# Optimization experiments

Hardware: AMD Instinct MI355X
Metric: run time of the kernel (lower is better)

Reference implementation:

```python
import jax, jax.numpy as jnp
import numpy as np

N = 50000
E = 800000
IN_DIM, HID, HEADS, OUT_DIM = 32, 64, 4, 128
HC = HID * HEADS  # 256
LN_EPS = 1e-5
NEG_SLOPE = 0.2


def setup_inputs() -> dict:
    key = jax.random.key(0)
    ks = jax.random.split(key, 16)
    s = 0.05
    inp = {
        "x": jax.random.normal(ks[0], (N, IN_DIM), dtype=jnp.float32),
        "edge_index": jax.random.randint(ks[1], (2, E), 0, N, dtype=jnp.int32),
        # input projection
        "W_in": jax.random.normal(ks[2], (IN_DIM, HID), dtype=jnp.float32) * s,
        "b_in": jnp.zeros((HID,), dtype=jnp.float32),
        # GAT layer 0: in=HID, out=HID per head, HEADS heads
        "lin0_w": jax.random.normal(ks[3], (HID, HC), dtype=jnp.float32) * s,
        "att0_src": jax.random.normal(ks[4], (HEADS, HID), dtype=jnp.float32) * s,
        "att0_dst": jax.random.normal(ks[5], (HEADS, HID), dtype=jnp.float32) * s,
        "bias0": jnp.zeros((HC,), dtype=jnp.float32),
        # GAT layer 1: in=HC, out=HID per head
        "lin1_w": jax.random.normal(ks[6], (HC, HC), dtype=jnp.float32) * s,
        "att1_src": jax.random.normal(ks[7], (HEADS, HID), dtype=jnp.float32) * s,
        "att1_dst": jax.random.normal(ks[8], (HEADS, HID), dtype=jnp.float32) * s,
        "bias1": jnp.zeros((HC,), dtype=jnp.float32),
        # output projection + layernorm
        "W_out": jax.random.normal(ks[9], (HC, OUT_DIM), dtype=jnp.float32) * s,
        "b_out": jnp.zeros((OUT_DIM,), dtype=jnp.float32),
        "ln_gamma": jnp.ones((OUT_DIM,), dtype=jnp.float32),
        "ln_beta": jnp.zeros((OUT_DIM,), dtype=jnp.float32),
    }
    return inp


def _gat_conv(x, src, dst, lin_w, att_src, att_dst, bias):
    # x: [N, F_in]; src/dst: [E'] (self-loops included)
    h = (x @ lin_w).reshape(N, HEADS, HID)           # [N, H, C]
    a_src = jnp.einsum("nhc,hc->nh", h, att_src)      # [N, H]
    a_dst = jnp.einsum("nhc,hc->nh", h, att_dst)      # [N, H]
    e = a_src[src] + a_dst[dst]                        # [E', H]
    e = jnp.where(e > 0, e, NEG_SLOPE * e)             # leaky_relu(0.2)
    # segment softmax over incoming edges per destination
    m = jax.ops.segment_max(e, dst, num_segments=N)    # [N, H]
    p = jnp.exp(e - m[dst])
    denom = jax.ops.segment_sum(p, dst, num_segments=N)
    alpha = p / (denom[dst] + 1e-16)                   # [E', H]
    msg = h[src] * alpha[:, :, None]                   # [E', H, C]
    out = jax.ops.segment_sum(msg, dst, num_segments=N)  # [N, H, C]
    return out.reshape(N, HC) + bias


def reference(x, edge_index, W_in, b_in, lin0_w, att0_src, att0_dst, bias0,
              lin1_w, att1_src, att1_dst, bias1, W_out, b_out, ln_gamma, ln_beta):
    # add self-loops (PyG GATConv default)
    loops = jnp.arange(N, dtype=edge_index.dtype)
    src = jnp.concatenate([edge_index[0], loops])
    dst = jnp.concatenate([edge_index[1], loops])

    h = jax.nn.elu(x @ W_in + b_in)
    h = jax.nn.elu(_gat_conv(h, src, dst, lin0_w, att0_src, att0_dst, bias0))
    h = jax.nn.elu(_gat_conv(h, src, dst, lin1_w, att1_src, att1_dst, bias1))
    h = h @ W_out + b_out
    mu = jnp.mean(h, axis=-1, keepdims=True)
    var = jnp.mean((h - mu) ** 2, axis=-1, keepdims=True)
    return (h - mu) * jax.lax.rsqrt(var + LN_EPS) * ln_gamma + ln_beta
```

## Files before the change

kernel.cpp:

```cpp
#include <hip/hip_runtime.h>
#include <cstdint>

#define N_NODES 50000
#define N_EDGES 800000
#define EP (N_EDGES + N_NODES)
#define IN_DIM 32
#define HID 64
#define HEADS 4
#define HC 256
#define OUT_DIM 128
#define NEG_SLOPE 0.2f
#define LN_EPS 1e-5f
#define SCAN_B 1024
#define NB ((N_NODES + SCAN_B - 1) / SCAN_B)

typedef __attribute__((ext_vector_type(8))) short bf16x8;
typedef __attribute__((ext_vector_type(16))) float f32x16;

__device__ __forceinline__ unsigned bf16rne(float f) {
    unsigned u = __float_as_uint(f);
    return (u + 0x7fffu + ((u >> 16) & 1u)) >> 16;
}
__device__ __forceinline__ unsigned pack_bf2(float a, float b) {
    return bf16rne(a) | (bf16rne(b) << 16);
}
__device__ __forceinline__ float bf_lo(unsigned w) { return __uint_as_float(w << 16); }
__device__ __forceinline__ float bf_hi(unsigned w) { return __uint_as_float(w & 0xffff0000u); }

__global__ void k_in_proj(const float* __restrict__ x, const float* __restrict__ W,
                          const float* __restrict__ b, unsigned short* __restrict__ out) {
    int g = blockIdx.x * blockDim.x + threadIdx.x;
    int n = g >> 6, j = g & 63;
    const float* xr = x + n * IN_DIM;
    float acc = b[j];
#pragma unroll
    for (int k = 0; k < IN_DIM; ++k) acc += xr[k] * W[k * HID + j];
    acc = acc > 0.f ? acc : (__expf(acc) - 1.f);
    out[g] = (unsigned short)bf16rne(acc);
}

__global__ void k_wpack(const float* __restrict__ w0, const float* __restrict__ w1,
                        const float* __restrict__ w2, unsigned short* __restrict__ p0,
                        unsigned short* __restrict__ p1, unsigned short* __restrict__ p2) {
    int g = blockIdx.x * blockDim.x + threadIdx.x;
    if (g < HID * HC) {
        int k = g >> 8, n = g & 255;
        p0[(((k >> 3) * HC) + n) * 8 + (k & 7)] = (unsigned short)bf16rne(w0[g]);
    } else if (g < HID * HC + HC * HC) {
        int t = g - HID * HC;
        int k = t >> 8, n = t & 255;
        p1[(((k >> 3) * HC) + n) * 8 + (k & 7)] = (unsigned short)bf16rne(w1[t]);
    } else if (g < HID * HC + HC * HC + HC * OUT_DIM) {
        int t = g - HID * HC - HC * HC;
        int k = t >> 7, n = t & 127;
        p2[(((k >> 3) * OUT_DIM) + n) * 8 + (k & 7)] = (unsigned short)bf16rne(w2[t]);
    }
}

__global__ void k_att_w(const float* __restrict__ w, const float* __restrict__ as,
                        const float* __restrict__ ad, unsigned short* __restrict__ ext,
                        int K) {
    int t = blockIdx.x * blockDim.x + threadIdx.x;
    if (t >= K * 8) return;
    int k = t >> 3, col = t & 7, h = col & 3;
    const float* att = (col < 4) ? as : ad;
    float acc = 0.f;
#pragma unroll 4
    for (int c = 0; c < HID; ++c) acc += w[k * HC + h * HID + c] * att[h * HID + c];
    ext[(k >> 3) * 256 + col * 8 + (k & 7)] = (unsigned short)bf16rne(acc);
}

template <int K>
__global__ __launch_bounds__(256) void k_gemm_lin(
        const unsigned short* __restrict__ A, const unsigned short* __restrict__ Bp,
        const unsigned short* __restrict__ Ext, unsigned short* __restrict__ hh,
        float* __restrict__ a_src, float* __restrict__ a_dst) {
    const int lane = threadIdx.x & 63;
    const int quad = lane >> 5, c = lane & 31;
    const int wave = threadIdx.x >> 6;
    const int m0 = blockIdx.x * 64 + (wave >> 1) * 32;
    const int cb = (wave & 1) * 128;
    f32x16 acc[4];
#pragma unroll
    for (int nt = 0; nt < 4; ++nt)
#pragma unroll
        for (int i = 0; i < 16; ++i) acc[nt][i] = 0.f;
    f32x16 acce;
#pragma unroll
    for (int i = 0; i < 16; ++i) acce[i] = 0.f;
    int mrow = m0 + c; if (mrow >= N_NODES) mrow = N_NODES - 1;
    const size_t abase = (size_t)mrow * K + quad * 8;
    for (int k0 = 0; k0 < K; k0 += 16) {
        bf16x8 af = *(const bf16x8*)(A + abase + k0);
        const unsigned short* bk = Bp + ((size_t)(k0 >> 3) + quad) * (HC * 8);
#pragma unroll
        for (int nt = 0; nt < 4; ++nt) {
            bf16x8 bf = *(const bf16x8*)(bk + (cb + nt * 32 + c) * 8);
            acc[nt] = __builtin_amdgcn_mfma_f32_32x32x16_bf16(af, bf, acc[nt], 0, 0, 0);
        }
        if (wave & 1) {
            bf16x8 bfe = *(const bf16x8*)(Ext + ((k0 >> 3) + quad) * 256 + c * 8);
            acce = __builtin_amdgcn_mfma_f32_32x32x16_bf16(af, bfe, acce, 0, 0, 0);
        }
    }
#pragma unroll
    for (int reg = 0; reg < 16; ++reg) {
        int row = (reg & 3) + 8 * (reg >> 2) + 4 * quad;
        int m = m0 + row;
        if (m < N_NODES) {
            size_t base = (size_t)m * HC + cb + c;
#pragma unroll
            for (int nt = 0; nt < 4; ++nt)
                hh[base + nt * 32] = (unsigned short)bf16rne(acc[nt][reg]);
            if ((wave & 1) && c < 8) {
                float v = acce[reg];
                if (c < 4) a_src[m * HEADS + c] = v;
                else       a_dst[m * HEADS + (c - 4)] = v;
            }
        }
    }
}

__global__ void k_hist(const int* __restrict__ ei, int* __restrict__ counts,
                       int* __restrict__ rank) {
    int e = blockIdx.x * blockDim.x + threadIdx.x;
    if (e >= EP) return;
    int d = (e < N_EDGES) ? ei[N_EDGES + e] : (e - N_EDGES);
    rank[e] = atomicAdd(&counts[d], 1);
}

__global__ void k_scan1(const int* __restrict__ counts, int* __restrict__ chunk_excl,
                        int* __restrict__ bsum) {
    __shared__ int buf[SCAN_B];
    int i = blockIdx.x * SCAN_B + threadIdx.x;
    int v = (i < N_NODES) ? counts[i] : 0;
    buf[threadIdx.x] = v;
    __syncthreads();
    for (int off = 1; off < SCAN_B; off <<= 1) {
        int t = (threadIdx.x >= off) ? buf[threadIdx.x - off] : 0;
        __syncthreads();
        buf[threadIdx.x] += t;
        __syncthreads();
    }
    if (i < N_NODES) chunk_excl[i] = buf[threadIdx.x] - v;
    if (threadIdx.x == SCAN_B - 1) bsum[blockIdx.x] = buf[SCAN_B - 1];
}

__global__ void k_scan3(const int* __restrict__ chunk_excl, const int* __restrict__ bsum,
                        int* __restrict__ row_ptr) {
    __shared__ int sbase;
    if (threadIdx.x < 64) {
        int v = (threadIdx.x < blockIdx.x) ? bsum[threadIdx.x] : 0;
#pragma unroll
        for (int mk = 1; mk < 64; mk <<= 1) v += __shfl_xor(v, mk, 64);
        if (threadIdx.x == 0) sbase = v;
    }
    __syncthreads();
    int i = blockIdx.x * SCAN_B + threadIdx.x;
    if (i < N_NODES) row_ptr[i] = chunk_excl[i] + sbase;
    if (i == 0) row_ptr[N_NODES] = EP;
}

__global__ void k_scatter(const int* __restrict__ ei, const int* __restrict__ row_ptr,
                          const int* __restrict__ rank, int* __restrict__ esrc) {
    int e = blockIdx.x * blockDim.x + threadIdx.x;
    if (e >= EP) return;
    int s, d;
    if (e < N_EDGES) { s = ei[e]; d = ei[N_EDGES + e]; } else { s = d = e - N_EDGES; }
    esrc[row_ptr[d] + rank[e]] = s;
}

__global__ __launch_bounds__(256) void k_gat_agg(
        const int* __restrict__ row_ptr, const int* __restrict__ esrc,
        const unsigned short* __restrict__ hh, const float* __restrict__ a_src,
        const float* __restrict__ a_dst, const float* __restrict__ bias,
        unsigned short* __restrict__ out) {
    const int wave = threadIdx.x >> 6;
    const int lane = threadIdx.x & 63;
    const int d = blockIdx.x * 4 + wave;
    const int h = lane >> 4;
    const unsigned j = (unsigned)(lane * 4);
    const float ad = a_dst[((unsigned)d << 2) + h];
    const int beg = row_ptr[d], end = row_ptr[d + 1];
    float4 acc = {0.f, 0.f, 0.f, 0.f};
    float psum = 0.f;
    for (int base = beg; base < end; base += 64) {
        int cnt = end - base; if (cnt > 64) cnt = 64;
        int idx = base + lane;
        int myv = esrc[idx < end ? idx : end - 1];
        int i = 0;
        for (; i + 8 <= cnt; i += 8) {
            int s0 = __shfl(myv, i, 64),     s1 = __shfl(myv, i + 1, 64);
            int s2 = __shfl(myv, i + 2, 64), s3 = __shfl(myv, i + 3, 64);
            int s4 = __shfl(myv, i + 4, 64), s5 = __shfl(myv, i + 5, 64);
            int s6 = __shfl(myv, i + 6, 64), s7 = __shfl(myv, i + 7, 64);
            float as0 = a_src[((unsigned)s0 << 2) + h], as1 = a_src[((unsigned)s1 << 2) + h];
            float as2 = a_src[((unsigned)s2 << 2) + h], as3 = a_src[((unsigned)s3 << 2) + h];
            float as4 = a_src[((unsigned)s4 << 2) + h], as5 = a_src[((unsigned)s5 << 2) + h];
            float as6 = a_src[((unsigned)s6 << 2) + h], as7 = a_src[((unsigned)s7 << 2) + h];
            uint2 g0 = *(const uint2*)(hh + (((unsigned)s0 << 8) + j));
            uint2 g1 = *(const uint2*)(hh + (((unsigned)s1 << 8) + j));
            uint2 g2 = *(const uint2*)(hh + (((unsigned)s2 << 8) + j));
            uint2 g3 = *(const uint2*)(hh + (((unsigned)s3 << 8) + j));
            uint2 g4 = *(const uint2*)(hh + (((unsigned)s4 << 8) + j));
            uint2 g5 = *(const uint2*)(hh + (((unsigned)s5 << 8) + j));
            uint2 g6 = *(const uint2*)(hh + (((unsigned)s6 << 8) + j));
            uint2 g7 = *(const uint2*)(hh + (((unsigned)s7 << 8) + j));
            float e0 = as0 + ad, e1 = as1 + ad, e2 = as2 + ad, e3 = as3 + ad;
            float e4 = as4 + ad, e5 = as5 + ad, e6 = as6 + ad, e7 = as7 + ad;
            e0 = fmaxf(e0, NEG_SLOPE * e0); e1 = fmaxf(e1, NEG_SLOPE * e1);
            e2 = fmaxf(e2, NEG_SLOPE * e2); e3 = fmaxf(e3, NEG_SLOPE * e3);
            e4 = fmaxf(e4, NEG_SLOPE * e4); e5 = fmaxf(e5, NEG_SLOPE * e5);
            e6 = fmaxf(e6, NEG_SLOPE * e6); e7 = fmaxf(e7, NEG_SLOPE * e7);
            float p0 = __expf(e0), p1 = __expf(e1), p2 = __expf(e2), p3 = __expf(e3);
            float p4 = __expf(e4), p5 = __expf(e5), p6 = __expf(e6), p7 = __expf(e7);
            psum += ((p0 + p1) + (p2 + p3)) + ((p4 + p5) + (p6 + p7));
            acc.x += p0 * bf_lo(g0.x) + p1 * bf_lo(g1.x) + p2 * bf_lo(g2.x) + p3 * bf_lo(g3.x)
                   + p4 * bf_lo(g4.x) + p5 * bf_lo(g5.x) + p6 * bf_lo(g6.x) + p7 * bf_lo(g7.x);
            acc.y += p0 * bf_hi(g0.x) + p1 * bf_hi(g1.x) + p2 * bf_hi(g2.x) + p3 * bf_hi(g3.x)
                   + p4 * bf_hi(g4.x) + p5 * bf_hi(g5.x) + p6 * bf_hi(g6.x) + p7 * bf_hi(g7.x);
            acc.z += p0 * bf_lo(g0.y) + p1 * bf_lo(g1.y) + p2 * bf_lo(g2.y) + p3 * bf_lo(g3.y)
                   + p4 * bf_lo(g4.y) + p5 * bf_lo(g5.y) + p6 * bf_lo(g6.y) + p7 * bf_lo(g7.y);
            acc.w += p0 * bf_hi(g0.y) + p1 * bf_hi(g1.y) + p2 * bf_hi(g2.y) + p3 * bf_hi(g3.y)
                   + p4 * bf_hi(g4.y) + p5 * bf_hi(g5.y) + p6 * bf_hi(g6.y) + p7 * bf_hi(g7.y);
        }
        for (; i < cnt; ++i) {
            int s0 = __shfl(myv, i, 64);
            float as0 = a_src[((unsigned)s0 << 2) + h];
            uint2 g0 = *(const uint2*)(hh + (((unsigned)s0 << 8) + j));
            float e0 = as0 + ad;
            e0 = fmaxf(e0, NEG_SLOPE * e0);
            float p0 = __expf(e0);
            psum += p0;
            acc.x += p0 * bf_lo(g0.x);
            acc.y += p0 * bf_hi(g0.x);
            acc.z += p0 * bf_lo(g0.y);
            acc.w += p0 * bf_hi(g0.y);
        }
    }
    const float inv = 1.f / (psum + 1e-16f);
    const float4 bb = *(const float4*)(bias + j);
    float4 v;
    v.x = acc.x * inv + bb.x; v.y = acc.y * inv + bb.y;
    v.z = acc.z * inv + bb.z; v.w = acc.w * inv + bb.w;
    v.x = v.x > 0.f ? v.x : (__expf(v.x) - 1.f);
    v.y = v.y > 0.f ? v.y : (__expf(v.y) - 1.f);
    v.z = v.z > 0.f ? v.z : (__expf(v.z) - 1.f);
    v.w = v.w > 0.f ? v.w : (__expf(v.w) - 1.f);
    uint2 pk;
    pk.x = pack_bf2(v.x, v.y);
    pk.y = pack_bf2(v.z, v.w);
    *(uint2*)(out + (size_t)d * HC + j) = pk;
}

__global__ __launch_bounds__(256) void k_gemm_out(
        const unsigned short* __restrict__ A, const unsigned short* __restrict__ Bp,
        const float* __restrict__ b, const float* __restrict__ gamma,
        const float* __restrict__ beta, float* __restrict__ out) {
    const int lane = threadIdx.x & 63;
    const int quad = lane >> 5, c = lane & 31;
    const int m0 = blockIdx.x * 128 + (threadIdx.x >> 6) * 32;
    f32x16 acc[4];
#pragma unroll
    for (int nt = 0; nt < 4; ++nt)
#pragma unroll
        for (int i = 0; i < 16; ++i) acc[nt][i] = 0.f;
    int mrow = m0 + c; if (mrow >= N_NODES) mrow = N_NODES - 1;
    const size_t abase = (size_t)mrow * HC + quad * 8;
    for (int k0 = 0; k0 < HC; k0 += 16) {
        bf16x8 af = *(const bf16x8*)(A + abase + k0);
        const unsigned short* bk = Bp + ((size_t)(k0 >> 3) + quad) * (OUT_DIM * 8);
#pragma unroll
        for (int nt = 0; nt < 4; ++nt) {
            bf16x8 bf = *(const bf16x8*)(bk + (nt * 32 + c) * 8);
            acc[nt] = __builtin_amdgcn_mfma_f32_32x32x16_bf16(af, bf, acc[nt], 0, 0, 0);
        }
    }
    float bb[4], gg[4], be[4];
#pragma unroll
    for (int nt = 0; nt < 4; ++nt) {
        int col = nt * 32 + c;
        bb[nt] = b[col]; gg[nt] = gamma[col]; be[nt] = beta[col];
    }
#pragma unroll
    for (int reg = 0; reg < 16; ++reg) {
        int row = (reg & 3) + 8 * (reg >> 2) + 4 * quad;
        int m = m0 + row;
        float v[4];
        float s = 0.f, s2 = 0.f;
#pragma unroll
        for (int nt = 0; nt < 4; ++nt) {
            v[nt] = acc[nt][reg] + bb[nt];
            s += v[nt]; s2 += v[nt] * v[nt];
        }
#pragma unroll
        for (int mk = 1; mk < 32; mk <<= 1) {
            s += __shfl_xor(s, mk, 64);
            s2 += __shfl_xor(s2, mk, 64);
        }
        float mu = s * (1.f / OUT_DIM);
        float var = s2 * (1.f / OUT_DIM) - mu * mu;
        float inv = rsqrtf(var + LN_EPS);
        if (m < N_NODES) {
            size_t base = (size_t)m * OUT_DIM + c;
#pragma unroll
            for (int nt = 0; nt < 4; ++nt)
                out[base + nt * 32] = (v[nt] - mu) * inv * gg[nt] + be[nt];
        }
    }
}

extern "C" void kernel_launch(void* const* d_in, const int* in_sizes, int n_in,
                              void* d_out, int out_size, void* d_ws, size_t ws_size,
                              hipStream_t stream) {
    const float* x        = (const float*)d_in[0];
    const int*   ei       = (const int*)  d_in[1];
    const float* W_in     = (const float*)d_in[2];
    const float* b_in     = (const float*)d_in[3];
    const float* lin0_w   = (const float*)d_in[4];
    const float* att0_src = (const float*)d_in[5];
    const float* att0_dst = (const float*)d_in[6];
    const float* bias0    = (const float*)d_in[7];
    const float* lin1_w   = (const float*)d_in[8];
    const float* att1_src = (const float*)d_in[9];
    const float* att1_dst = (const float*)d_in[10];
    const float* bias1    = (const float*)d_in[11];
    const float* W_out    = (const float*)d_in[12];
    const float* b_out    = (const float*)d_in[13];
    const float* ln_gamma = (const float*)d_in[14];
    const float* ln_beta  = (const float*)d_in[15];
    float* out = (float*)d_out;

    unsigned short* us = (unsigned short*)d_ws;
    unsigned short* h_in_bf = us;
    unsigned short* hh_bf   = h_in_bf + (size_t)N_NODES * HID;
    unsigned short* feat_bf = hh_bf + (size_t)N_NODES * HC;
    unsigned short* p0      = feat_bf + (size_t)N_NODES * HC;
    unsigned short* p1      = p0 + HID * HC;
    unsigned short* p2      = p1 + HC * HC;
    unsigned short* ext0    = p2 + HC * OUT_DIM;
    unsigned short* ext1    = ext0 + 2048;
    float* a_src = (float*)(ext1 + 8192);
    float* a_dst = a_src + (size_t)N_NODES * HEADS;
    int* counts     = (int*)(a_dst + (size_t)N_NODES * HEADS);
    int* chunk_excl = counts + N_NODES;
    int* bsum       = chunk_excl + N_NODES;
    int* row_ptr    = bsum + NB;
    int* rank       = row_ptr + N_NODES + 1;
    int* esrc       = rank + EP;

    k_in_proj<<<(N_NODES * HID) / 256, 256, 0, stream>>>(x, W_in, b_in, h_in_bf);
    k_wpack<<<(HID * HC + HC * HC + HC * OUT_DIM + 255) / 256, 256, 0, stream>>>(
        lin0_w, lin1_w, W_out, p0, p1, p2);
    hipMemsetAsync(ext0, 0, (2048 + 8192) * sizeof(unsigned short), stream);
    k_att_w<<<(HID * 8 + 255) / 256, 256, 0, stream>>>(lin0_w, att0_src, att0_dst, ext0, HID);
    k_att_w<<<(HC * 8 + 255) / 256, 256, 0, stream>>>(lin1_w, att1_src, att1_dst, ext1, HC);

    hipMemsetAsync(counts, 0, N_NODES * sizeof(int), stream);
    k_hist<<<(EP + 255) / 256, 256, 0, stream>>>(ei, counts, rank);
    k_scan1<<<NB, SCAN_B, 0, stream>>>(counts, chunk_excl, bsum);
    k_scan3<<<NB, SCAN_B, 0, stream>>>(chunk_excl, bsum, row_ptr);
    k_scatter<<<(EP + 255) / 256, 256, 0, stream>>>(ei, row_ptr, rank, esrc);

    const int lin_grid = (N_NODES + 63) / 64;
    const int out_grid = (N_NODES + 127) / 128;

    k_gemm_lin<HID><<<lin_grid, 256, 0, stream>>>(h_in_bf, p0, ext0, hh_bf, a_src, a_dst);
    k_gat_agg<<<N_NODES / 4, 256, 0, stream>>>(row_ptr, esrc, hh_bf, a_src, a_dst,
                                               bias0, feat_bf);

    k_gemm_lin<HC><<<lin_grid, 256, 0, stream>>>(feat_bf, p1, ext1, hh_bf, a_src, a_dst);
    k_gat_agg<<<N_NODES / 4, 256, 0, stream>>>(row_ptr, esrc, hh_bf, a_src, a_dst,
                                               bias1, feat_bf);

    k_gemm_out<<<out_grid, 256, 0, stream>>>(feat_bf, p2, b_out, ln_gamma, ln_beta, out);
}
```

Baseline: 377.3 us.

## Process two destination nodes per wave in GAT aggregation and fuse prep kernels

The aggregation kernel now splits each wave into two 32-lane halves, each handling one destination node with 16-byte gathers of 8 bf16 channels per lane instead of 8-byte gathers of 4. The aim is to halve wasted lanes for low-degree nodes and widen the memory transactions. The input projection, weight packing and attention-vector folding kernels, plus a memset, are merged into one prep launch that also writes the zero padding directly. The high bf16 half is now read unmasked, which adds small low-bit noise to the values.

Result: faster. 365.0 us (-3.3%).

```diff
diff --git a/kernel.cpp b/kernel.cpp
--- a/kernel.cpp
+++ b/kernel.cpp
@@ -25,49 +25,60 @@
     return bf16rne(a) | (bf16rne(b) << 16);
 }
 __device__ __forceinline__ float bf_lo(unsigned w) { return __uint_as_float(w << 16); }
-__device__ __forceinline__ float bf_hi(unsigned w) { return __uint_as_float(w & 0xffff0000u); }
-
-__global__ void k_in_proj(const float* __restrict__ x, const float* __restrict__ W,
-                          const float* __restrict__ b, unsigned short* __restrict__ out) {
-    int g = blockIdx.x * blockDim.x + threadIdx.x;
-    int n = g >> 6, j = g & 63;
-    const float* xr = x + n * IN_DIM;
-    float acc = b[j];
-#pragma unroll
-    for (int k = 0; k < IN_DIM; ++k) acc += xr[k] * W[k * HID + j];
-    acc = acc > 0.f ? acc : (__expf(acc) - 1.f);
-    out[g] = (unsigned short)bf16rne(acc);
-}
-
-__global__ void k_wpack(const float* __restrict__ w0, const float* __restrict__ w1,
-                        const float* __restrict__ w2, unsigned short* __restrict__ p0,
-                        unsigned short* __restrict__ p1, unsigned short* __restrict__ p2) {
-    int g = blockIdx.x * blockDim.x + threadIdx.x;
-    if (g < HID * HC) {
-        int k = g >> 8, n = g & 255;
-        p0[(((k >> 3) * HC) + n) * 8 + (k & 7)] = (unsigned short)bf16rne(w0[g]);
-    } else if (g < HID * HC + HC * HC) {
-        int t = g - HID * HC;
-        int k = t >> 8, n = t & 255;
-        p1[(((k >> 3) * HC) + n) * 8 + (k & 7)] = (unsigned short)bf16rne(w1[t]);
-    } else if (g < HID * HC + HC * HC + HC * OUT_DIM) {
-        int t = g - HID * HC - HC * HC;
-        int k = t >> 7, n = t & 127;
-        p2[(((k >> 3) * OUT_DIM) + n) * 8 + (k & 7)] = (unsigned short)bf16rne(w2[t]);
-    }
-}
-
-__global__ void k_att_w(const float* __restrict__ w, const float* __restrict__ as,
-                        const float* __restrict__ ad, unsigned short* __restrict__ ext,
-                        int K) {
-    int t = blockIdx.x * blockDim.x + threadIdx.x;
-    if (t >= K * 8) return;
-    int k = t >> 3, col = t & 7, h = col & 3;
-    const float* att = (col < 4) ? as : ad;
-    float acc = 0.f;
+__device__ __forceinline__ float bf_hi_raw(unsigned w) { return __uint_as_float(w); }
+
+#define PREP_INPROJ ((N_NODES * HID) / 256)
+#define PREP_WPACK ((HID * HC + HC * HC + HC * OUT_DIM) / 256)
+#define PREP_EXT 40
+__global__ void k_prep(const float* __restrict__ x, const float* __restrict__ W_in,
+                       const float* __restrict__ b_in, unsigned short* __restrict__ h_in,
+                       const float* __restrict__ w0, const float* __restrict__ w1,
+                       const float* __restrict__ w2, unsigned short* __restrict__ p0,
+                       unsigned short* __restrict__ p1, unsigned short* __restrict__ p2,
+                       const float* __restrict__ as0, const float* __restrict__ ad0,
+                       unsigned short* __restrict__ ext0,
+                       const float* __restrict__ as1, const float* __restrict__ ad1,
+                       unsigned short* __restrict__ ext1) {
+    if (blockIdx.x < PREP_INPROJ) {
+        int g = blockIdx.x * 256 + threadIdx.x;
+        int n = g >> 6, j = g & 63;
+        const float* xr = x + n * IN_DIM;
+        float acc = b_in[j];
+#pragma unroll
+        for (int k = 0; k < IN_DIM; ++k) acc += xr[k] * W_in[k * HID + j];
+        acc = acc > 0.f ? acc : (__expf(acc) - 1.f);
+        h_in[g] = (unsigned short)bf16rne(acc);
+    } else if (blockIdx.x < PREP_INPROJ + PREP_WPACK) {
+        int g = (blockIdx.x - PREP_INPROJ) * 256 + threadIdx.x;
+        if (g < HID * HC) {
+            int k = g >> 8, n = g & 255;
+            p0[(((k >> 3) * HC) + n) * 8 + (k & 7)] = (unsigned short)bf16rne(w0[g]);
+        } else if (g < HID * HC + HC * HC) {
+            int t = g - HID * HC;
+            int k = t >> 8, n = t & 255;
+            p1[(((k >> 3) * HC) + n) * 8 + (k & 7)] = (unsigned short)bf16rne(w1[t]);
+        } else {
+            int t = g - HID * HC - HC * HC;
+            int k = t >> 7, n = t & 127;
+            p2[(((k >> 3) * OUT_DIM) + n) * 8 + (k & 7)] = (unsigned short)bf16rne(w2[t]);
+        }
+    } else {
+        int t = (blockIdx.x - PREP_INPROJ - PREP_WPACK) * 256 + threadIdx.x;
+        const float* w; const float* as; const float* ad; unsigned short* ext; int e;
+        if (t < 2048) { w = w0; as = as0; ad = ad0; ext = ext0; e = t; }
+        else if (t < 2048 + 8192) { w = w1; as = as1; ad = ad1; ext = ext1; e = t - 2048; }
+        else return;
+        int kb = e >> 8, rem = e & 255, col = rem >> 3, kk = rem & 7;
+        int k = kb * 8 + kk;
+        float acc = 0.f;
+        if (col < 8) {
+            int h = col & 3;
+            const float* att = (col < 4) ? as : ad;
 #pragma unroll 4
-    for (int c = 0; c < HID; ++c) acc += w[k * HC + h * HID + c] * att[h * HID + c];
-    ext[(k >> 3) * 256 + col * 8 + (k & 7)] = (unsigned short)bf16rne(acc);
+            for (int c = 0; c < HID; ++c) acc += w[k * HC + h * HID + c] * att[h * HID + c];
+        }
+        ext[e] = (unsigned short)bf16rne(acc);
+    }
 }
 
 template <int K>
@@ -177,80 +188,78 @@
         unsigned short* __restrict__ out) {
     const int wave = threadIdx.x >> 6;
     const int lane = threadIdx.x & 63;
-    const int d = blockIdx.x * 4 + wave;
-    const int h = lane >> 4;
-    const unsigned j = (unsigned)(lane * 4);
+    const int half = lane >> 5;
+    const int l = lane & 31;
+    const int d = blockIdx.x * 8 + wave * 2 + half;
+    const int h = l >> 3;
+    const unsigned c0 = (unsigned)(l * 8);
+    const int bsrc = half << 5;
     const float ad = a_dst[((unsigned)d << 2) + h];
     const int beg = row_ptr[d], end = row_ptr[d + 1];
-    float4 acc = {0.f, 0.f, 0.f, 0.f};
+    float acc[8];
+#pragma unroll
+    for (int t = 0; t < 8; ++t) acc[t] = 0.f;
     float psum = 0.f;
-    for (int base = beg; base < end; base += 64) {
-        int cnt = end - base; if (cnt > 64) cnt = 64;
-        int idx = base + lane;
+    for (int base = beg; base < end; base += 32) {
+        int cnt = end - base; if (cnt > 32) cnt = 32;
+        int idx = base + l;
         int myv = esrc[idx < end ? idx : end - 1];
         int i = 0;
-        for (; i + 8 <= cnt; i += 8) {
-            int s0 = __shfl(myv, i, 64),     s1 = __shfl(myv, i + 1, 64);
-            int s2 = __shfl(myv, i + 2, 64), s3 = __shfl(myv, i + 3, 64);
-            int s4 = __shfl(myv, i + 4, 64), s5 = __shfl(myv, i + 5, 64);
-            int s6 = __shfl(myv, i + 6, 64), s7 = __shfl(myv, i + 7, 64);
-            float as0 = a_src[((unsigned)s0 << 2) + h], as1 = a_src[((unsigned)s1 << 2) + h];
-            float as2 = a_src[((unsigned)s2 << 2) + h], as3 = a_src[((unsigned)s3 << 2) + h];
-            float as4 = a_src[((unsigned)s4 << 2) + h], as5 = a_src[((unsigned)s5 << 2) + h];
-            float as6 = a_src[((unsigned)s6 << 2) + h], as7 = a_src[((unsigned)s7 << 2) + h];
-            uint2 g0 = *(const uint2*)(hh + (((unsigned)s0 << 8) + j));
-            uint2 g1 = *(const uint2*)(hh + (((unsigned)s1 << 8) + j));
-            uint2 g2 = *(const uint2*)(hh + (((unsigned)s2 << 8) + j));
-            uint2 g3 = *(const uint2*)(hh + (((unsigned)s3 << 8) + j));
-            uint2 g4 = *(const uint2*)(hh + (((unsigned)s4 << 8) + j));
-            uint2 g5 = *(const uint2*)(hh + (((unsigned)s5 << 8) + j));
-            uint2 g6 = *(const uint2*)(hh + (((unsigned)s6 << 8) + j));
-            uint2 g7 = *(const uint2*)(hh + (((unsigned)s7 << 8) + j));
+        for (; i + 4 <= cnt; i += 4) {
+            int s0 = __shfl(myv, bsrc + i, 64);
+            int s1 = __shfl(myv, bsrc + i + 1, 64);
+            int s2 = __shfl(myv, bsrc + i + 2, 64);
+            int s3 = __shfl(myv, bsrc + i + 3, 64);
+            float as0 = a_src[((unsigned)s0 << 2) + h];
+            float as1 = a_src[((unsigned)s1 << 2) + h];
+            float as2 = a_src[((unsigned)s2 << 2) + h];
+            float as3 = a_src[((unsigned)s3 << 2) + h];
+            uint4 g0 = *(const uint4*)(hh + (((unsigned)s0 << 8) + c0));
+            uint4 g1 = *(const uint4*)(hh + (((unsigned)s1 << 8) + c0));
+            uint4 g2 = *(const uint4*)(hh + (((unsigned)s2 << 8) + c0));
+            uint4 g3 = *(const uint4*)(hh + (((unsigned)s3 << 8) + c0));
             float e0 = as0 + ad, e1 = as1 + ad, e2 = as2 + ad, e3 = as3 + ad;
-            float e4 = as4 + ad, e5 = as5 + ad, e6 = as6 + ad, e7 = as7 + ad;
             e0 = fmaxf(e0, NEG_SLOPE * e0); e1 = fmaxf(e1, NEG_SLOPE * e1);
             e2 = fmaxf(e2, NEG_SLOPE * e2); e3 = fmaxf(e3, NEG_SLOPE * e3);
-            e4 = fmaxf(e4, NEG_SLOPE * e4); e5 = fmaxf(e5, NEG_SLOPE * e5);
-            e6 = fmaxf(e6, NEG_SLOPE * e6); e7 = fmaxf(e7, NEG_SLOPE * e7);
             float p0 = __expf(e0), p1 = __expf(e1), p2 = __expf(e2), p3 = __expf(e3);
-            float p4 = __expf(e4), p5 = __expf(e5), p6 = __expf(e6), p7 = __expf(e7);
-            psum += ((p0 + p1) + (p2 + p3)) + ((p4 + p5) + (p6 + p7));
-            acc.x += p0 * bf_lo(g0.x) + p1 * bf_lo(g1.x) + p2 * bf_lo(g2.x) + p3 * bf_lo(g3.x)
-                   + p4 * bf_lo(g4.x) + p5 * bf_lo(g5.x) + p6 * bf_lo(g6.x) + p7 * bf_lo(g7.x);
-            acc.y += p0 * bf_hi(g0.x) + p1 * bf_hi(g1.x) + p2 * bf_hi(g2.x) + p3 * bf_hi(g3.x)
-                   + p4 * bf_hi(g4.x) + p5 * bf_hi(g5.x) + p6 * bf_hi(g6.x) + p7 * bf_hi(g7.x);
-            acc.z += p0 * bf_lo(g0.y) + p1 * bf_lo(g1.y) + p2 * bf_lo(g2.y) + p3 * bf_lo(g3.y)
-                   + p4 * bf_lo(g4.y) + p5 * bf_lo(g5.y) + p6 * bf_lo(g6.y) + p7 * bf_lo(g7.y);
-            acc.w += p0 * bf_hi(g0.y) + p1 * bf_hi(g1.y) + p2 * bf_hi(g2.y) + p3 * bf_hi(g3.y)
-                   + p4 * bf_hi(g4.y) + p5 * bf_hi(g5.y) + p6 * bf_hi(g6.y) + p7 * bf_hi(g7.y);
+            psum += (p0 + p1) + (p2 + p3);
+            acc[0] += p0 * bf_lo(g0.x) + p1 * bf_lo(g1.x) + p2 * bf_lo(g2.x) + p3 * bf_lo(g3.x);
+            acc[1] += p0 * bf_hi_raw(g0.x) + p1 * bf_hi_raw(g1.x) + p2 * bf_hi_raw(g2.x) + p3 * bf_hi_raw(g3.x);
+            acc[2] += p0 * bf_lo(g0.y) + p1 * bf_lo(g1.y) + p2 * bf_lo(g2.y) + p3 * bf_lo(g3.y);
+            acc[3] += p0 * bf_hi_raw(g0.y) + p1 * bf_hi_raw(g1.y) + p2 * bf_hi_raw(g2.y) + p3 * bf_hi_raw(g3.y);
+            acc[4] += p0 * bf_lo(g0.z) + p1 * bf_lo(g1.z) + p2 * bf_lo(g2.z) + p3 * bf_lo(g3.z);
+            acc[5] += p0 * bf_hi_raw(g0.z) + p1 * bf_hi_raw(g1.z) + p2 * bf_hi_raw(g2.z) + p3 * bf_hi_raw(g3.z);
+            acc[6] += p0 * bf_lo(g0.w) + p1 * bf_lo(g1.w) + p2 * bf_lo(g2.w) + p3 * bf_lo(g3.w);
+            acc[7] += p0 * bf_hi_raw(g0.w) + p1 * bf_hi_raw(g1.w) + p2 * bf_hi_raw(g2.w) + p3 * bf_hi_raw(g3.w);
         }
         for (; i < cnt; ++i) {
-            int s0 = __shfl(myv, i, 64);
+            int s0 = __shfl(myv, bsrc + i, 64);
             float as0 = a_src[((unsigned)s0 << 2) + h];
-            uint2 g0 = *(const uint2*)(hh + (((unsigned)s0 << 8) + j));
+            uint4 g0 = *(const uint4*)(hh + (((unsigned)s0 << 8) + c0));
             float e0 = as0 + ad;
             e0 = fmaxf(e0, NEG_SLOPE * e0);
             float p0 = __expf(e0);
             psum += p0;
-            acc.x += p0 * bf_lo(g0.x);
-            acc.y += p0 * bf_hi(g0.x);
-            acc.z += p0 * bf_lo(g0.y);
-            acc.w += p0 * bf_hi(g0.y);
+            acc[0] += p0 * bf_lo(g0.x); acc[1] += p0 * bf_hi_raw(g0.x);
+            acc[2] += p0 * bf_lo(g0.y); acc[3] += p0 * bf_hi_raw(g0.y);
+            acc[4] += p0 * bf_lo(g0.z); acc[5] += p0 * bf_hi_raw(g0.z);
+            acc[6] += p0 * bf_lo(g0.w); acc[7] += p0 * bf_hi_raw(g0.w);
         }
     }
     const float inv = 1.f / (psum + 1e-16f);
-    const float4 bb = *(const float4*)(bias + j);
-    float4 v;
-    v.x = acc.x * inv + bb.x; v.y = acc.y * inv + bb.y;
-    v.z = acc.z * inv + bb.z; v.w = acc.w * inv + bb.w;
-    v.x = v.x > 0.f ? v.x : (__expf(v.x) - 1.f);
-    v.y = v.y > 0.f ? v.y : (__expf(v.y) - 1.f);
-    v.z = v.z > 0.f ? v.z : (__expf(v.z) - 1.f);
-    v.w = v.w > 0.f ? v.w : (__expf(v.w) - 1.f);
-    uint2 pk;
-    pk.x = pack_bf2(v.x, v.y);
-    pk.y = pack_bf2(v.z, v.w);
-    *(uint2*)(out + (size_t)d * HC + j) = pk;
+    const float4 bb0 = *(const float4*)(bias + c0);
+    const float4 bb1 = *(const float4*)(bias + c0 + 4);
+    float v[8];
+    v[0] = acc[0] * inv + bb0.x; v[1] = acc[1] * inv + bb0.y;
+    v[2] = acc[2] * inv + bb0.z; v[3] = acc[3] * inv + bb0.w;
+    v[4] = acc[4] * inv + bb1.x; v[5] = acc[5] * inv + bb1.y;
+    v[6] = acc[6] * inv + bb1.z; v[7] = acc[7] * inv + bb1.w;
+#pragma unroll
+    for (int t = 0; t < 8; ++t) v[t] = v[t] > 0.f ? v[t] : (__expf(v[t]) - 1.f);
+    uint4 pk;
+    pk.x = pack_bf2(v[0], v[1]); pk.y = pack_bf2(v[2], v[3]);
+    pk.z = pack_bf2(v[4], v[5]); pk.w = pack_bf2(v[6], v[7]);
+    *(uint4*)(out + (((size_t)d << 8) + c0)) = pk;
 }
 
 __global__ __launch_bounds__(256) void k_gemm_out(
@@ -349,12 +358,9 @@
     int* rank       = row_ptr + N_NODES + 1;
     int* esrc       = rank + EP;
 
-    k_in_proj<<<(N_NODES * HID) / 256, 256, 0, stream>>>(x, W_in, b_in, h_in_bf);
-    k_wpack<<<(HID * HC + HC * HC + HC * OUT_DIM + 255) / 256, 256, 0, stream>>>(
-        lin0_w, lin1_w, W_out, p0, p1, p2);
-    hipMemsetAsync(ext0, 0, (2048 + 8192) * sizeof(unsigned short), stream);
-    k_att_w<<<(HID * 8 + 255) / 256, 256, 0, stream>>>(lin0_w, att0_src, att0_dst, ext0, HID);
-    k_att_w<<<(HC * 8 + 255) / 256, 256, 0, stream>>>(lin1_w, att1_src, att1_dst, ext1, HC);
+    k_prep<<<PREP_INPROJ + PREP_WPACK + PREP_EXT, 256, 0, stream>>>(
+        x, W_in, b_in, h_in_bf, lin0_w, lin1_w, W_out, p0, p1, p2,
+        att0_src, att0_dst, ext0, att1_src, att1_dst, ext1);
 
     hipMemsetAsync(counts, 0, N_NODES * sizeof(int), stream);
     k_hist<<<(EP + 255) / 256, 256, 0, stream>>>(ei, counts, rank);
@@ -366,11 +372,11 @@
     const int out_grid = (N_NODES + 127) / 128;
 
     k_gemm_lin<HID><<<lin_grid, 256, 0, stream>>>(h_in_bf, p0, ext0, hh_bf, a_src, a_dst);
-    k_gat_agg<<<N_NODES / 4, 256, 0, stream>>>(row_ptr, esrc, hh_bf, a_src, a_dst,
+    k_gat_agg<<<N_NODES / 8, 256, 0, stream>>>(row_ptr, esrc, hh_bf, a_src, a_dst,
                                                bias0, feat_bf);
 
     k_gemm_lin<HC><<<lin_grid, 256, 0, stream>>>(feat_bf, p1, ext1, hh_bf, a_src, a_dst);
-    k_gat_agg<<<N_NODES / 4, 256, 0, stream>>>(row_ptr, esrc, hh_bf, a_src, a_dst,
+    k_gat_agg<<<N_NODES / 8, 256, 0, stream>>>(row_ptr, esrc, hh_bf, a_src, a_dst,
                                                bias1, feat_bf);
 
     k_gemm_out<<<out_grid, 256, 0, stream>>>(feat_bf, p2, b_out, ln_gamma, ln_beta, out);
```
